# Optimization experiments

Hardware: AMD Instinct MI355X
Metric: run time of the kernel (lower is better)

The kernel has to match this reference:

```python
import jax, jax.numpy as jnp
import numpy as np

N = 100_000        # nodes
E = 3_200_000      # edges (avg degree 32)
D_IN = 512
D_HID = 512
D_OUT = 512
EPS = 1e-5         # BatchNorm1d eps


def _xavier(key, fan_out, fan_in, gain=1.414):
    a = gain * np.sqrt(6.0 / (fan_in + fan_out))
    return jax.random.uniform(key, (fan_out, fan_in), jnp.float32, -a, a)


def setup_inputs() -> dict:
    key = jax.random.key(0)
    ks = jax.random.split(key, 6)
    graph_node = jax.random.normal(ks[0], (N, D_IN), jnp.float32)
    edge_index = jax.random.randint(ks[1], (2, E), 0, N, dtype=jnp.int32)
    return {
        "graph_node": graph_node,
        "edge_index": edge_index,
        "W0": _xavier(ks[2], D_HID, D_IN),
        "b0": jnp.zeros((D_HID,), jnp.float32),
        "W1": _xavier(ks[3], D_HID, D_HID),
        "b1": jnp.zeros((D_HID,), jnp.float32),
        "W2": _xavier(ks[4], D_OUT, D_HID),
        "b2": jnp.zeros((D_OUT,), jnp.float32),
    }


def _gcn_scale(src, dst):
    # Faithful to torch gcn_conv: self-loops removed then re-added for all N
    # nodes; degree computed on dst; edge messages h[src]*w are scattered to
    # src (the cols tensor in the original is dead code). Hence the whole op
    # reduces to a per-node scale s[i] = sum_{out-edges of i} w + deg[i]^-1.
    mask = (src != dst).astype(jnp.float32)          # drop self-loops
    deg = jax.ops.segment_sum(mask, dst, num_segments=N) + 1.0  # +1 self-loop
    dinv = deg ** -0.5                               # deg >= 1, no inf
    w = dinv[src] * dinv[dst] * mask                 # [E]
    s = jax.ops.segment_sum(w, src, num_segments=N) + 1.0 / deg  # [N]
    return s


def _batchnorm(x):
    # BatchNorm1d(affine=False, track_running_stats=False): batch stats always
    mu = x.mean(axis=0)
    var = x.var(axis=0)  # biased variance, matches torch normalization
    return (x - mu) * jax.lax.rsqrt(var + EPS)


def reference(graph_node, edge_index, W0, b0, W1, b1, W2, b2):
    src, dst = edge_index[0], edge_index[1]
    s = _gcn_scale(src, dst)[:, None]                # [N,1], graph-only
    x = graph_node
    for W, b in ((W0, b0), (W1, b1)):
        x = (x @ W.T) * s + b                        # linear, gcn_conv, bias
        x = jax.nn.relu(_batchnorm(x))
        # dropout inactive at inference
    x = (x @ W2.T) * s + b2
    return x
```

## Files before the change

kernel.cpp:

```cpp
#include <hip/hip_runtime.h>

#define N_NODES 100000
#define N_EDGES 3200000
#define DIM 512
#define MPAD 100096
#define MTILES 782
#define BN_EPS 1e-5f

#define RBITS 14
#define NBINS 16384
#define NRANGE 8
#define NBLK 64
#define EDGES_PER_BLK (N_EDGES / NBLK)

typedef _Float16 half8 __attribute__((ext_vector_type(8)));
typedef float floatx4 __attribute__((ext_vector_type(4)));


__global__ __launch_bounds__(256) void convert_x_kernel(const float* __restrict__ x,
                                                        _Float16* __restrict__ out) {
    size_t idx = ((size_t)blockIdx.x * 256 + threadIdx.x) * 8;
    int row = (int)(idx >> 9);
    half8 h;
    if (row < N_NODES) {
        const float4* p = (const float4*)(x + idx);
        float4 a = p[0], b = p[1];
        h[0] = (_Float16)a.x; h[1] = (_Float16)a.y; h[2] = (_Float16)a.z; h[3] = (_Float16)a.w;
        h[4] = (_Float16)b.x; h[5] = (_Float16)b.y; h[6] = (_Float16)b.z; h[7] = (_Float16)b.w;
    } else {
        #pragma unroll
        for (int k = 0; k < 8; ++k) h[k] = (_Float16)0.0f;
    }
    *(half8*)(out + idx) = h;
}

__global__ __launch_bounds__(256) void convert_w_kernel(const float* __restrict__ in,
                                                        _Float16* __restrict__ out) {
    size_t idx = ((size_t)blockIdx.x * 256 + threadIdx.x) * 8;
    const float4* p = (const float4*)(in + idx);
    float4 a = p[0], b = p[1];
    half8 h;
    h[0] = (_Float16)a.x; h[1] = (_Float16)a.y; h[2] = (_Float16)a.z; h[3] = (_Float16)a.w;
    h[4] = (_Float16)b.x; h[5] = (_Float16)b.y; h[6] = (_Float16)b.z; h[7] = (_Float16)b.w;
    *(half8*)(out + idx) = h;
}


template <bool IS_DEG>
__global__ __launch_bounds__(256) void hist_stage1(const int* __restrict__ ei,
                                                   const float* __restrict__ dinv,
                                                   float* __restrict__ part) {
    __shared__ float bins[NBINS];
    const int tid = threadIdx.x;
    const int r = blockIdx.x & (NRANGE - 1);
    const int b = blockIdx.x >> 3;
    for (int i = tid; i < NBINS; i += 256) bins[i] = 0.f;
    __syncthreads();

    const int e0 = b * EDGES_PER_BLK;
    const int e1 = e0 + EDGES_PER_BLK;
    const int lo = r << RBITS;
    const int hi = lo + NBINS;
    for (int e = e0 + tid * 4; e < e1; e += 256 * 4) {
        int4 sv = *(const int4*)(ei + e);
        int4 dv = *(const int4*)(ei + N_EDGES + e);
        const int ss[4] = {sv.x, sv.y, sv.z, sv.w};
        const int dd[4] = {dv.x, dv.y, dv.z, dv.w};
        #pragma unroll
        for (int k = 0; k < 4; ++k) {
            const int s = ss[k], d = dd[k];
            if (s == d) continue;
            const int key = IS_DEG ? d : s;
            if (key >= lo && key < hi) {
                const float val = IS_DEG ? 1.0f : dinv[d];
                atomicAdd(&bins[key - lo], val);
            }
        }
    }
    __syncthreads();

    float* dst = part + (size_t)blockIdx.x * NBINS;
    for (int i = tid; i < NBINS; i += 256) dst[i] = bins[i];
}

__global__ __launch_bounds__(256) void hist_stage2_deg(const float* __restrict__ part,
                                                       float* __restrict__ dinv,
                                                       float* __restrict__ sarr) {
    const int i = blockIdx.x * 256 + threadIdx.x;
    if (i >= MPAD) return;
    const int r = i >> RBITS, bin = i & (NBINS - 1);
    float h = 0.f;
    #pragma unroll 8
    for (int b = 0; b < NBLK; ++b)
        h += part[(size_t)(b * NRANGE + r) * NBINS + bin];
    if (i < N_NODES) {
        const float deg = h + 1.0f;
        dinv[i] = rsqrtf(deg);
        sarr[i] = 1.0f / deg;
    } else {
        dinv[i] = 0.f;
        sarr[i] = 0.f;
    }
}

__global__ __launch_bounds__(256) void hist_stage2_s(const float* __restrict__ part,
                                                     const float* __restrict__ dinv,
                                                     float* __restrict__ sarr) {
    const int i = blockIdx.x * 256 + threadIdx.x;
    if (i >= MPAD) return;
    const int r = i >> RBITS, bin = i & (NBINS - 1);
    float t = 0.f;
    #pragma unroll 8
    for (int b = 0; b < NBLK; ++b)
        t += part[(size_t)(b * NRANGE + r) * NBINS + bin];
    if (i < N_NODES) sarr[i] += dinv[i] * t;
}


template <bool FINAL>
__global__ __launch_bounds__(256) void gemm_kernel(
    const _Float16* __restrict__ A,
    const _Float16* __restrict__ W,
    const float* __restrict__ sarr,
    const float* __restrict__ bias,
    void* __restrict__ out,
    float* __restrict__ colsum,
    float* __restrict__ colsq)
{
    __shared__ _Float16 As[128 * 32];
    __shared__ _Float16 Bs[128 * 32];
    __shared__ float lsum[128];
    __shared__ float lsq[128];

    const int tid  = threadIdx.x;
    const int wave = tid >> 6;
    const int lane = tid & 63;
    const int quad = lane >> 4;
    const int l16  = lane & 15;

    const int ct = blockIdx.x & 3;
    const int rt = blockIdx.x >> 2;
    const int m0 = rt * 128;
    const int n0 = ct * 128;
    const int wm = (wave >> 1) * 64;
    const int wn = (wave & 1) * 64;

    floatx4 acc[4][4];
    #pragma unroll
    for (int i = 0; i < 4; ++i)
        #pragma unroll
        for (int j = 0; j < 4; ++j)
            acc[i][j] = (floatx4){0.f, 0.f, 0.f, 0.f};

    const int f0 = wave * 1024 + lane * 16;
    const int ra = f0 >> 6;
    const int ca = f0 & 63;

    const char* Ab = (const char*)(A + (size_t)m0 * DIM) + ca;
    const char* Bb = (const char*)(W + (size_t)n0 * DIM) + ca;

    for (int kb = 0; kb < DIM; kb += 32) {
        #pragma unroll
        for (int is = 0; is < 2; ++is) {
            int r = is * 64 + ra;
            __builtin_amdgcn_global_load_lds(
                (const __attribute__((address_space(1))) void*)(Ab + (size_t)r * (DIM * 2) + kb * 2),
                (__attribute__((address_space(3))) void*)(As + is * 2048 + (f0 >> 1)),
                16, 0, 0);
            __builtin_amdgcn_global_load_lds(
                (const __attribute__((address_space(1))) void*)(Bb + (size_t)r * (DIM * 2) + kb * 2),
                (__attribute__((address_space(3))) void*)(Bs + is * 2048 + (f0 >> 1)),
                16, 0, 0);
        }
        __syncthreads();

        half8 af[4], bfr[4];
        #pragma unroll
        for (int i = 0; i < 4; ++i)
            af[i] = *(const half8*)(As + (wm + i * 16 + l16) * 32 + quad * 8);
        #pragma unroll
        for (int j = 0; j < 4; ++j)
            bfr[j] = *(const half8*)(Bs + (wn + j * 16 + l16) * 32 + quad * 8);

        #pragma unroll
        for (int i = 0; i < 4; ++i)
            #pragma unroll
            for (int j = 0; j < 4; ++j)
                acc[i][j] = __builtin_amdgcn_mfma_f32_16x16x32_f16(af[i], bfr[j], acc[i][j], 0, 0, 0);

        __syncthreads();
    }

    if (!FINAL) {
        if (tid < 128) { lsum[tid] = 0.f; lsq[tid] = 0.f; }
        __syncthreads();
    }

    float4 sva[4];
    #pragma unroll
    for (int i = 0; i < 4; ++i)
        sva[i] = *(const float4*)(sarr + m0 + wm + i * 16 + quad * 4);
    float bv[4];
    #pragma unroll
    for (int j = 0; j < 4; ++j)
        bv[j] = bias[n0 + wn + j * 16 + l16];

    #pragma unroll
    for (int j = 0; j < 4; ++j) {
        const int col_g = n0 + wn + j * 16 + l16;
        float cs = 0.f, cq = 0.f;
        #pragma unroll
        for (int i = 0; i < 4; ++i) {
            const int rbase = m0 + wm + i * 16 + quad * 4;
            #pragma unroll
            for (int r = 0; r < 4; ++r) {
                const int row_g = rbase + r;
                const float sval = ((const float*)&sva[i])[r];
                const float yv = acc[i][j][r] * sval + bv[j];
                if (FINAL) {
                    if (row_g < N_NODES)
                        ((float*)out)[(size_t)row_g * DIM + col_g] = yv;
                } else {
                    ((_Float16*)out)[(size_t)row_g * DIM + col_g] = (_Float16)yv;
                    if (row_g < N_NODES) { cs += yv; cq += yv * yv; }
                }
            }
        }
        if (!FINAL) {
            atomicAdd(&lsum[wn + j * 16 + l16], cs);
            atomicAdd(&lsq[wn + j * 16 + l16], cq);
        }
    }
    if (!FINAL) {
        __syncthreads();
        if (tid < 128) {
            atomicAdd(&colsum[n0 + tid], lsum[tid]);
            atomicAdd(&colsq[n0 + tid], lsq[tid]);
        }
    }
}


__global__ void bn_finalize(const float* __restrict__ colsum, const float* __restrict__ colsq,
                            float* __restrict__ mu, float* __restrict__ rstd) {
    int c = threadIdx.x;
    float m = colsum[c] * (1.0f / (float)N_NODES);
    float v = colsq[c] * (1.0f / (float)N_NODES) - m * m;
    mu[c] = m;
    rstd[c] = rsqrtf(v + BN_EPS);
}

__global__ __launch_bounds__(256) void bn_apply(_Float16* __restrict__ y,
                                                const float* __restrict__ mu,
                                                const float* __restrict__ rstd) {
    size_t idx = ((size_t)blockIdx.x * 256 + threadIdx.x) * 8;
    int row = (int)(idx >> 9);
    int col = (int)(idx & 511);
    half8 h;
    if (row < N_NODES) {
        h = *(const half8*)(y + idx);
        float4 m0 = *(const float4*)(mu + col);
        float4 m1 = *(const float4*)(mu + col + 4);
        float4 r0 = *(const float4*)(rstd + col);
        float4 r1 = *(const float4*)(rstd + col + 4);
        float mus[8] = {m0.x, m0.y, m0.z, m0.w, m1.x, m1.y, m1.z, m1.w};
        float rs[8]  = {r0.x, r0.y, r0.z, r0.w, r1.x, r1.y, r1.z, r1.w};
        #pragma unroll
        for (int k = 0; k < 8; ++k) {
            float v = ((float)h[k] - mus[k]) * rs[k];
            h[k] = (_Float16)fmaxf(v, 0.f);
        }
    } else {
        #pragma unroll
        for (int k = 0; k < 8; ++k) h[k] = (_Float16)0.0f;
    }
    *(half8*)(y + idx) = h;
}


extern "C" void kernel_launch(void* const* d_in, const int* in_sizes, int n_in,
                              void* d_out, int out_size, void* d_ws, size_t ws_size,
                              hipStream_t stream) {
    const float* graph_node = (const float*)d_in[0];
    const int*   edge_index = (const int*)d_in[1];
    const float* W0 = (const float*)d_in[2];
    const float* b0 = (const float*)d_in[3];
    const float* W1 = (const float*)d_in[4];
    const float* b1 = (const float*)d_in[5];
    const float* W2 = (const float*)d_in[6];
    const float* b2 = (const float*)d_in[7];

    char* ws = (char*)d_ws;
    const size_t XB = (size_t)MPAD * DIM * 2;
    _Float16* x0  = (_Float16*)ws;
    _Float16* wf  = (_Float16*)(ws + XB);
    float* dinv   = (float*)(ws + XB + 3 * DIM * DIM * 2);
    float* sarr   = dinv + MPAD;
    float* stats  = sarr + MPAD;
    float *sum0 = stats,        *sq0 = stats + 512,  *mu0 = stats + 1024, *rstd0 = stats + 1536;
    float *sum1 = stats + 2048, *sq1 = stats + 2560, *mu1 = stats + 3072, *rstd1 = stats + 3584;

    _Float16* x1 = (_Float16*)d_out;
    float* part = (float*)((char*)d_out + (size_t)110 * 1024 * 1024);

    hipMemsetAsync(stats, 0, 4096 * sizeof(float), stream);

    const int elemBlocks = MPAD * DIM / 8 / 256;
    convert_x_kernel<<<elemBlocks, 256, 0, stream>>>(graph_node, x0);
    convert_w_kernel<<<128, 256, 0, stream>>>(W0, wf);
    convert_w_kernel<<<128, 256, 0, stream>>>(W1, wf + 262144);
    convert_w_kernel<<<128, 256, 0, stream>>>(W2, wf + 524288);

    const int statBlocks = (MPAD + 255) / 256;
    hist_stage1<true><<<NRANGE * NBLK, 256, 0, stream>>>(edge_index, dinv, part);
    hist_stage2_deg<<<statBlocks, 256, 0, stream>>>(part, dinv, sarr);
    hist_stage1<false><<<NRANGE * NBLK, 256, 0, stream>>>(edge_index, dinv, part);
    hist_stage2_s<<<statBlocks, 256, 0, stream>>>(part, dinv, sarr);

    gemm_kernel<false><<<MTILES * 4, 256, 0, stream>>>(x0, wf, sarr, b0, x1, sum0, sq0);
    bn_finalize<<<1, 512, 0, stream>>>(sum0, sq0, mu0, rstd0);
    bn_apply<<<elemBlocks, 256, 0, stream>>>(x1, mu0, rstd0);

    gemm_kernel<false><<<MTILES * 4, 256, 0, stream>>>(x1, wf + 262144, sarr, b1, x0, sum1, sq1);
    bn_finalize<<<1, 512, 0, stream>>>(sum1, sq1, mu1, rstd1);
    bn_apply<<<elemBlocks, 256, 0, stream>>>(x0, mu1, rstd1);

    gemm_kernel<true><<<MTILES * 4, 256, 0, stream>>>(x0, wf + 524288, sarr, b2, d_out,
                                                      nullptr, nullptr);
}
```

Measured before the change: 938.5 us.

## Double-buffer GEMM LDS tiles and remap workgroup IDs across XCDs

The GEMM main loop now uses two LDS buffers, so the next K-slice is fetched with global_load_lds while MFMAs run on the current one, which halves the barriers per iteration. Workgroup indices in both the GEMM and the histogram kernel are permuted so that consecutive tiles land on the same XCD, improving L2 locality for the shared weight and edge data. The cost is double the LDS footprint, which may lower occupancy, and the remap assumes grid sizes divisible by 8.

```diff
diff --git a/kernel.cpp b/kernel.cpp
--- a/kernel.cpp
+++ b/kernel.cpp
@@ -52,8 +52,9 @@
                                                    float* __restrict__ part) {
     __shared__ float bins[NBINS];
     const int tid = threadIdx.x;
-    const int r = blockIdx.x & (NRANGE - 1);
-    const int b = blockIdx.x >> 3;
+    const int wg = (blockIdx.x & 7) * (NRANGE * NBLK / 8) + (blockIdx.x >> 3);
+    const int r = wg & (NRANGE - 1);
+    const int b = wg >> 3;
     for (int i = tid; i < NBINS; i += 256) bins[i] = 0.f;
     __syncthreads();
 
@@ -79,7 +80,7 @@
     }
     __syncthreads();
 
-    float* dst = part + (size_t)blockIdx.x * NBINS;
+    float* dst = part + (size_t)wg * NBINS;
     for (int i = tid; i < NBINS; i += 256) dst[i] = bins[i];
 }
 
@@ -127,8 +128,8 @@
     float* __restrict__ colsum,
     float* __restrict__ colsq)
 {
-    __shared__ _Float16 As[128 * 32];
-    __shared__ _Float16 Bs[128 * 32];
+    __shared__ _Float16 As[2][128 * 32];
+    __shared__ _Float16 Bs[2][128 * 32];
     __shared__ float lsum[128];
     __shared__ float lsq[128];
 
@@ -138,8 +139,9 @@
     const int quad = lane >> 4;
     const int l16  = lane & 15;
 
-    const int ct = blockIdx.x & 3;
-    const int rt = blockIdx.x >> 2;
+    const int wg = (blockIdx.x & 7) * (MTILES * 4 / 8) + (blockIdx.x >> 3);
+    const int ct = wg & 3;
+    const int rt = wg >> 2;
     const int m0 = rt * 128;
     const int n0 = ct * 128;
     const int wm = (wave >> 1) * 64;
@@ -159,37 +161,53 @@
     const char* Ab = (const char*)(A + (size_t)m0 * DIM) + ca;
     const char* Bb = (const char*)(W + (size_t)n0 * DIM) + ca;
 
-    for (int kb = 0; kb < DIM; kb += 32) {
+    auto stage = [&](int buf, int kb) {
         #pragma unroll
         for (int is = 0; is < 2; ++is) {
-            int r = is * 64 + ra;
+            const int r = is * 64 + ra;
             __builtin_amdgcn_global_load_lds(
                 (const __attribute__((address_space(1))) void*)(Ab + (size_t)r * (DIM * 2) + kb * 2),
-                (__attribute__((address_space(3))) void*)(As + is * 2048 + (f0 >> 1)),
+                (__attribute__((address_space(3))) void*)(&As[buf][is * 2048 + (f0 >> 1)]),
                 16, 0, 0);
             __builtin_amdgcn_global_load_lds(
                 (const __attribute__((address_space(1))) void*)(Bb + (size_t)r * (DIM * 2) + kb * 2),
-                (__attribute__((address_space(3))) void*)(Bs + is * 2048 + (f0 >> 1)),
+                (__attribute__((address_space(3))) void*)(&Bs[buf][is * 2048 + (f0 >> 1)]),
                 16, 0, 0);
         }
-        __syncthreads();
-
+    };
+
+    auto compute = [&](int buf) {
         half8 af[4], bfr[4];
         #pragma unroll
         for (int i = 0; i < 4; ++i)
-            af[i] = *(const half8*)(As + (wm + i * 16 + l16) * 32 + quad * 8);
+            af[i] = *(const half8*)(&As[buf][(wm + i * 16 + l16) * 32 + quad * 8]);
         #pragma unroll
         for (int j = 0; j < 4; ++j)
-            bfr[j] = *(const half8*)(Bs + (wn + j * 16 + l16) * 32 + quad * 8);
-
+            bfr[j] = *(const half8*)(&Bs[buf][(wn + j * 16 + l16) * 32 + quad * 8]);
         #pragma unroll
         for (int i = 0; i < 4; ++i)
             #pragma unroll
             for (int j = 0; j < 4; ++j)
                 acc[i][j] = __builtin_amdgcn_mfma_f32_16x16x32_f16(af[i], bfr[j], acc[i][j], 0, 0, 0);
-
+    };
+
+    stage(0, 0);
+    __syncthreads();
+
+    int kb = 32;
+    for (int it = 0; it < 7; ++it) {
+        stage(1, kb);
+        compute(0);
         __syncthreads();
-    }
+        stage(0, kb + 32);
+        compute(1);
+        __syncthreads();
+        kb += 64;
+    }
+    stage(1, kb);
+    compute(0);
+    __syncthreads();
+    compute(1);
 
     if (!FINAL) {
         if (tid < 128) { lsum[tid] = 0.f; lsq[tid] = 0.f; }
```

After: 903.2 us. -3.8%, faster.

## Rewrite GEMM as 256x256 double-buffered pipelined tile with XCD-aware block mapping

Applied to the files above, without the earlier changes.

Replaces the 128x128 single-buffered GEMM with a 512-thread, 256x256 tile kernel that double-buffers K-slices in LDS and interleaves async global-to-LDS loads with MFMA phases, using explicit waitcnt, barriers and setprio. LDS reads use an XOR swizzle to avoid bank conflicts, and workgroups are remapped so consecutive tiles land on the same XCD for L2 reuse. The histogram kernel also gets an XCD-aware block remap. The aim is to hide memory latency and raise MFMA utilisation, at the cost of higher register and LDS pressure and fragile hand-tuned scheduling.

```diff
diff --git a/kernel.cpp b/kernel.cpp
--- a/kernel.cpp
+++ b/kernel.cpp
@@ -4,8 +4,10 @@
 #define N_EDGES 3200000
 #define DIM 512
 #define MPAD 100096
-#define MTILES 782
 #define BN_EPS 1e-5f
+
+#define GRTILES 391
+#define GGRID 782
 
 #define RBITS 14
 #define NBINS 16384
@@ -52,8 +54,9 @@
                                                    float* __restrict__ part) {
     __shared__ float bins[NBINS];
     const int tid = threadIdx.x;
-    const int r = blockIdx.x & (NRANGE - 1);
-    const int b = blockIdx.x >> 3;
+    const int wg = (blockIdx.x & 7) * (NRANGE * NBLK / 8) + (blockIdx.x >> 3);
+    const int r = wg & (NRANGE - 1);
+    const int b = wg >> 3;
     for (int i = tid; i < NBINS; i += 256) bins[i] = 0.f;
     __syncthreads();
 
@@ -79,7 +82,7 @@
     }
     __syncthreads();
 
-    float* dst = part + (size_t)blockIdx.x * NBINS;
+    float* dst = part + (size_t)wg * NBINS;
     for (int i = tid; i < NBINS; i += 256) dst[i] = bins[i];
 }
 
@@ -117,8 +120,70 @@
 }
 
 
+#define BARRIER __builtin_amdgcn_s_barrier()
+#define WAIT_LGKM do { asm volatile("s_waitcnt lgkmcnt(0)" ::: "memory"); \
+                       __builtin_amdgcn_sched_barrier(0); } while (0)
+#define VM2 do { asm volatile("s_waitcnt vmcnt(2)" ::: "memory"); \
+                 __builtin_amdgcn_sched_barrier(0); } while (0)
+#define VM0 do { asm volatile("s_waitcnt vmcnt(0)" ::: "memory"); \
+                 __builtin_amdgcn_sched_barrier(0); } while (0)
+#define VM8 do { asm volatile("s_waitcnt vmcnt(8)" ::: "memory"); \
+                 __builtin_amdgcn_sched_barrier(0); } while (0)
+#define VNONE ((void)0)
+#define PRIO1 __builtin_amdgcn_s_setprio(1)
+#define PRIO0 __builtin_amdgcn_s_setprio(0)
+
+#define STG(buf, ab, h, kt) do { \
+    const char* _s = (ab) ? Bsrc : Asrc; \
+    __builtin_amdgcn_global_load_lds( \
+        (const __attribute__((address_space(1))) void*)(_s + (size_t)((h)*128 + rowS0)*1024 + (kt)*128 + cbS), \
+        (__attribute__((address_space(3))) void*)(&smem[buf][ab][h][tid*8]), 16, 0, 0); \
+    __builtin_amdgcn_global_load_lds( \
+        (const __attribute__((address_space(1))) void*)(_s + (size_t)((h)*128 + rowS0 + 64)*1024 + (kt)*128 + cbS), \
+        (__attribute__((address_space(3))) void*)(&smem[buf][ab][h][4096 + tid*8]), 16, 0, 0); \
+} while (0)
+
+#define RDA(base, i0) do { \
+    _Pragma("unroll") for (int ii = 0; ii < 4; ++ii) \
+        _Pragma("unroll") for (int s = 0; s < 2; ++s) \
+            fa[ii][s] = *(const half8*)((const char*)(base) + ((i0) + ii) * 2048 + s * 1024 + inb); \
+} while (0)
+
+#define RDB(base, j0) do { \
+    _Pragma("unroll") for (int jj = 0; jj < 2; ++jj) \
+        _Pragma("unroll") for (int s = 0; s < 2; ++s) \
+            fb[(j0) + jj][s] = *(const half8*)((const char*)(base) + (brow0 + (j0) + jj) * 2048 + s * 1024 + inb); \
+} while (0)
+
+#define MM(i0, j0) do { \
+    _Pragma("unroll") for (int s = 0; s < 2; ++s) \
+        _Pragma("unroll") for (int ii = 0; ii < 4; ++ii) \
+            _Pragma("unroll") for (int jj = 0; jj < 2; ++jj) \
+                acc[(i0)+ii][(j0)+jj] = __builtin_amdgcn_mfma_f32_16x16x32_f16( \
+                    fa[ii][s], fb[(j0)+jj][s], acc[(i0)+ii][(j0)+jj], 0, 0, 0); \
+} while (0)
+
+#define ITER(S13, S47, S8, KTA, KTB, KTC, VMP4, VMP8) do { \
+     RDA(Ab0, 0); RDB(Bb0, 0); if (S13) STG(1, 0, 1, KTA); \
+              BARRIER; WAIT_LGKM; PRIO1; MM(0, 0); PRIO0; BARRIER; \
+     RDB(Bb0, 2); if (S13) STG(1, 1, 0, KTA); \
+              BARRIER; WAIT_LGKM; PRIO1; MM(0, 2); PRIO0; BARRIER; \
+     RDA(Ab0, 4); if (S13) STG(1, 1, 1, KTA); \
+              BARRIER; WAIT_LGKM; PRIO1; MM(4, 0); PRIO0; BARRIER; \
+     if (S47) STG(0, 0, 0, KTB); \
+              BARRIER; PRIO1; MM(4, 2); PRIO0; VMP4; BARRIER; \
+     RDA(Ab1, 0); RDB(Bb1, 0); if (S47) STG(0, 0, 1, KTB); \
+              BARRIER; WAIT_LGKM; PRIO1; MM(0, 0); PRIO0; BARRIER; \
+     RDB(Bb1, 2); if (S47) STG(0, 1, 0, KTB); \
+              BARRIER; WAIT_LGKM; PRIO1; MM(0, 2); PRIO0; BARRIER; \
+     RDA(Ab1, 4); if (S47) STG(0, 1, 1, KTB); \
+              BARRIER; WAIT_LGKM; PRIO1; MM(4, 0); PRIO0; BARRIER; \
+     if (S8) STG(1, 0, 0, KTC); \
+              BARRIER; PRIO1; MM(4, 2); PRIO0; VMP8; BARRIER; \
+} while (0)
+
 template <bool FINAL>
-__global__ __launch_bounds__(256) void gemm_kernel(
+__global__ __launch_bounds__(512, 2) void gemm_kernel(
     const _Float16* __restrict__ A,
     const _Float16* __restrict__ W,
     const float* __restrict__ sarr,
@@ -127,10 +192,7 @@
     float* __restrict__ colsum,
     float* __restrict__ colsq)
 {
-    __shared__ _Float16 As[128 * 32];
-    __shared__ _Float16 Bs[128 * 32];
-    __shared__ float lsum[128];
-    __shared__ float lsq[128];
+    __shared__ _Float16 smem[2][2][2][8192];
 
     const int tid  = threadIdx.x;
     const int wave = tid >> 6;
@@ -138,85 +200,75 @@
     const int quad = lane >> 4;
     const int l16  = lane & 15;
 
-    const int ct = blockIdx.x & 3;
-    const int rt = blockIdx.x >> 2;
-    const int m0 = rt * 128;
-    const int n0 = ct * 128;
-    const int wm = (wave >> 1) * 64;
-    const int wn = (wave & 1) * 64;
-
-    floatx4 acc[4][4];
+    const int xcd = blockIdx.x & 7, bidx = blockIdx.x >> 3;
+    const int qq = 97, rr = 6;
+    const int wg = (xcd < rr ? xcd * (qq + 1) : rr * (qq + 1) + (xcd - rr) * qq) + bidx;
+    const int ct = wg & 1, rt = wg >> 1;
+    const int m0 = rt * 256, n0 = ct * 256;
+
+    const int wmh   = wave >> 2;
+    const int wnq   = wave & 3;
+    const int bhalf = (wave >> 1) & 1;
+    const int brow0 = (wave & 1) * 4;
+
+    const _Float16* Ab0 = &smem[0][0][wmh][0];
+    const _Float16* Ab1 = &smem[1][0][wmh][0];
+    const _Float16* Bb0 = &smem[0][1][bhalf][0];
+    const _Float16* Bb1 = &smem[1][1][bhalf][0];
+
+    const int inb = (l16 * 64 + quad * 16) ^ (((l16 >> 3) & 1) << 5);
+
+    const int st0 = tid >> 6;
+    int bsw = (tid & 63) * 16;
+    bsw ^= ((bsw >> 9) & 1) << 5;
+    const int rowS0 = ((st0 >> 1) << 4) + (bsw >> 6);
+    const int cbS   = ((st0 & 1) << 6) + (bsw & 63);
+
+    const char* Asrc = (const char*)(A + (size_t)m0 * DIM);
+    const char* Bsrc = (const char*)(W + (size_t)n0 * DIM);
+
+    floatx4 acc[8][4];
     #pragma unroll
-    for (int i = 0; i < 4; ++i)
+    for (int i = 0; i < 8; ++i)
         #pragma unroll
         for (int j = 0; j < 4; ++j)
             acc[i][j] = (floatx4){0.f, 0.f, 0.f, 0.f};
 
-    const int f0 = wave * 1024 + lane * 16;
-    const int ra = f0 >> 6;
-    const int ca = f0 & 63;
-
-    const char* Ab = (const char*)(A + (size_t)m0 * DIM) + ca;
-    const char* Bb = (const char*)(W + (size_t)n0 * DIM) + ca;
-
-    for (int kb = 0; kb < DIM; kb += 32) {
-        #pragma unroll
-        for (int is = 0; is < 2; ++is) {
-            int r = is * 64 + ra;
-            __builtin_amdgcn_global_load_lds(
-                (const __attribute__((address_space(1))) void*)(Ab + (size_t)r * (DIM * 2) + kb * 2),
-                (__attribute__((address_space(3))) void*)(As + is * 2048 + (f0 >> 1)),
-                16, 0, 0);
-            __builtin_amdgcn_global_load_lds(
-                (const __attribute__((address_space(1))) void*)(Bb + (size_t)r * (DIM * 2) + kb * 2),
-                (__attribute__((address_space(3))) void*)(Bs + is * 2048 + (f0 >> 1)),
-                16, 0, 0);
-        }
+    half8 fa[4][2];
+    half8 fb[4][2];
+
+    STG(0, 0, 0, 0); STG(0, 0, 1, 0); STG(0, 1, 0, 0); STG(0, 1, 1, 0);
+    STG(1, 0, 0, 1); STG(1, 0, 1, 1); STG(1, 1, 0, 1); STG(1, 1, 1, 1);
+    VM8;
+    BARRIER;
+
+    ITER(false, true,  true,  1, 2, 3, VM2, VM2);
+    ITER(true,  true,  true,  3, 4, 5, VM2, VM2);
+    ITER(true,  true,  true,  5, 6, 7, VM2, VM2);
+    ITER(true,  false, false, 7, 0, 0, VM0, VNONE);
+
+    float* lsum = (float*)&smem[0][0][0][0];
+    float* lsq  = lsum + 256;
+    if (!FINAL) {
+        if (tid < 256) { lsum[tid] = 0.f; lsq[tid] = 0.f; }
         __syncthreads();
-
-        half8 af[4], bfr[4];
-        #pragma unroll
-        for (int i = 0; i < 4; ++i)
-            af[i] = *(const half8*)(As + (wm + i * 16 + l16) * 32 + quad * 8);
-        #pragma unroll
-        for (int j = 0; j < 4; ++j)
-            bfr[j] = *(const half8*)(Bs + (wn + j * 16 + l16) * 32 + quad * 8);
-
-        #pragma unroll
-        for (int i = 0; i < 4; ++i)
-            #pragma unroll
-            for (int j = 0; j < 4; ++j)
-                acc[i][j] = __builtin_amdgcn_mfma_f32_16x16x32_f16(af[i], bfr[j], acc[i][j], 0, 0, 0);
-
-        __syncthreads();
-    }
-
-    if (!FINAL) {
-        if (tid < 128) { lsum[tid] = 0.f; lsq[tid] = 0.f; }
-        __syncthreads();
-    }
-
-    float4 sva[4];
-    #pragma unroll
-    for (int i = 0; i < 4; ++i)
-        sva[i] = *(const float4*)(sarr + m0 + wm + i * 16 + quad * 4);
-    float bv[4];
-    #pragma unroll
-    for (int j = 0; j < 4; ++j)
-        bv[j] = bias[n0 + wn + j * 16 + l16];
-
+    }
+
+    const int crow0 = m0 + wmh * 128;
+    const int ccol0 = n0 + wnq * 64;
     #pragma unroll
     for (int j = 0; j < 4; ++j) {
-        const int col_g = n0 + wn + j * 16 + l16;
+        const int col_g = ccol0 + j * 16 + l16;
+        const float bv = bias[col_g];
         float cs = 0.f, cq = 0.f;
         #pragma unroll
-        for (int i = 0; i < 4; ++i) {
-            const int rbase = m0 + wm + i * 16 + quad * 4;
+        for (int i = 0; i < 8; ++i) {
+            const int rbase = crow0 + i * 16 + quad * 4;
+            const float4 sv = *(const float4*)(sarr + rbase);
             #pragma unroll
-            for (int r = 0; r < 4; ++r) {
-                const int row_g = rbase + r;
-                const float sval = ((const float*)&sva[i])[r];
-                const float yv = acc[i][j][r] * sval + bv[j];
+            for (int r2 = 0; r2 < 4; ++r2) {
+                const int row_g = rbase + r2;
+                const float yv = acc[i][j][r2] * ((const float*)&sv)[r2] + bv;
                 if (FINAL) {
                     if (row_g < N_NODES)
                         ((float*)out)[(size_t)row_g * DIM + col_g] = yv;
@@ -227,13 +279,13 @@
             }
         }
         if (!FINAL) {
-            atomicAdd(&lsum[wn + j * 16 + l16], cs);
-            atomicAdd(&lsq[wn + j * 16 + l16], cq);
+            atomicAdd(&lsum[wnq * 64 + j * 16 + l16], cs);
+            atomicAdd(&lsq[wnq * 64 + j * 16 + l16], cq);
         }
     }
     if (!FINAL) {
         __syncthreads();
-        if (tid < 128) {
+        if (tid < 256) {
             atomicAdd(&colsum[n0 + tid], lsum[tid]);
             atomicAdd(&colsq[n0 + tid], lsq[tid]);
         }
@@ -317,14 +369,14 @@
     hist_stage1<false><<<NRANGE * NBLK, 256, 0, stream>>>(edge_index, dinv, part);
     hist_stage2_s<<<statBlocks, 256, 0, stream>>>(part, dinv, sarr);
 
-    gemm_kernel<false><<<MTILES * 4, 256, 0, stream>>>(x0, wf, sarr, b0, x1, sum0, sq0);
+    gemm_kernel<false><<<GGRID, 512, 0, stream>>>(x0, wf, sarr, b0, x1, sum0, sq0);
     bn_finalize<<<1, 512, 0, stream>>>(sum0, sq0, mu0, rstd0);
     bn_apply<<<elemBlocks, 256, 0, stream>>>(x1, mu0, rstd0);
 
-    gemm_kernel<false><<<MTILES * 4, 256, 0, stream>>>(x1, wf + 262144, sarr, b1, x0, sum1, sq1);
+    gemm_kernel<false><<<GGRID, 512, 0, stream>>>(x1, wf + 262144, sarr, b1, x0, sum1, sq1);
     bn_finalize<<<1, 512, 0, stream>>>(sum1, sq1, mu1, rstd1);
     bn_apply<<<elemBlocks, 256, 0, stream>>>(x0, mu1, rstd1);
 
-    gemm_kernel<true><<<MTILES * 4, 256, 0, stream>>>(x0, wf + 524288, sarr, b2, d_out,
-                                                      nullptr, nullptr);
-}
+    gemm_kernel<true><<<GGRID, 512, 0, stream>>>(x0, wf + 524288, sarr, b2, d_out,
+                                                 nullptr, nullptr);
+}
```

Measured after the change: 857.1 us. -8.7%, faster.

## Restructure GEMM to keep weight slab in LDS and stream A from global

Applied to the files above, without the earlier changes.

The GEMM now uses 512-thread blocks covering a 512x64 output tile. Each block loads the full 64x512 weight slice into swizzled LDS once, and every wave reads its A fragments directly from global memory with no per-k-step LDS staging or barriers. Block IDs are remapped so that consecutive blocks spread across XCDs, in both the GEMM and the histogram kernels. This removes the per-iteration __syncthreads and A staging, but A loads from global are now uncoalesced-ish fragment reads, each A row tile is re-read by 8 column blocks, and the large LDS footprint limits occupancy.

```diff
diff --git a/kernel.cpp b/kernel.cpp
--- a/kernel.cpp
+++ b/kernel.cpp
@@ -4,8 +4,13 @@
 #define N_EDGES 3200000
 #define DIM 512
 #define MPAD 100096
-#define MTILES 782
 #define BN_EPS 1e-5f
+
+#define GBM 512
+#define GBN 64
+#define GMT 196
+#define GNT 8
+#define GGRID (GMT * GNT)
 
 #define RBITS 14
 #define NBINS 16384
@@ -52,8 +57,9 @@
                                                    float* __restrict__ part) {
     __shared__ float bins[NBINS];
     const int tid = threadIdx.x;
-    const int r = blockIdx.x & (NRANGE - 1);
-    const int b = blockIdx.x >> 3;
+    const int wg = (blockIdx.x & 7) * (NRANGE * NBLK / 8) + (blockIdx.x >> 3);
+    const int r = wg & (NRANGE - 1);
+    const int b = wg >> 3;
     for (int i = tid; i < NBINS; i += 256) bins[i] = 0.f;
     __syncthreads();
 
@@ -79,7 +85,7 @@
     }
     __syncthreads();
 
-    float* dst = part + (size_t)blockIdx.x * NBINS;
+    float* dst = part + (size_t)wg * NBINS;
     for (int i = tid; i < NBINS; i += 256) dst[i] = bins[i];
 }
 
@@ -118,7 +124,7 @@
 
 
 template <bool FINAL>
-__global__ __launch_bounds__(256) void gemm_kernel(
+__global__ __launch_bounds__(512, 4) void gemm_kernel(
     const _Float16* __restrict__ A,
     const _Float16* __restrict__ W,
     const float* __restrict__ sarr,
@@ -127,10 +133,9 @@
     float* __restrict__ colsum,
     float* __restrict__ colsq)
 {
-    __shared__ _Float16 As[128 * 32];
-    __shared__ _Float16 Bs[128 * 32];
-    __shared__ float lsum[128];
-    __shared__ float lsq[128];
+    __shared__ _Float16 Wl[GBN * DIM];
+    __shared__ float lsum[GBN];
+    __shared__ float lsq[GBN];
 
     const int tid  = threadIdx.x;
     const int wave = tid >> 6;
@@ -138,12 +143,24 @@
     const int quad = lane >> 4;
     const int l16  = lane & 15;
 
-    const int ct = blockIdx.x & 3;
-    const int rt = blockIdx.x >> 2;
-    const int m0 = rt * 128;
-    const int n0 = ct * 128;
-    const int wm = (wave >> 1) * 64;
-    const int wn = (wave & 1) * 64;
+    const int wg = (blockIdx.x & 7) * GMT + (blockIdx.x >> 3);
+    const int ct = wg & 7;
+    const int rt = wg >> 3;
+    const int m0 = rt * GBM;
+    const int n0 = ct * GBN;
+
+    {
+        const char* Wsrc = (const char*)(W + (size_t)n0 * DIM);
+        const int inswz = (lane * 16) ^ (wave << 4);
+        #pragma unroll
+        for (int it = 0; it < 8; ++it) {
+            __builtin_amdgcn_global_load_lds(
+                (const __attribute__((address_space(1))) void*)(Wsrc + (it * 8 + wave) * 1024 + inswz),
+                (__attribute__((address_space(3))) void*)(Wl + it * 4096 + tid * 8),
+                16, 0, 0);
+        }
+    }
+    __syncthreads();
 
     floatx4 acc[4][4];
     #pragma unroll
@@ -152,88 +169,66 @@
         for (int j = 0; j < 4; ++j)
             acc[i][j] = (floatx4){0.f, 0.f, 0.f, 0.f};
 
-    const int f0 = wave * 1024 + lane * 16;
-    const int ra = f0 >> 6;
-    const int ca = f0 & 63;
-
-    const char* Ab = (const char*)(A + (size_t)m0 * DIM) + ca;
-    const char* Bb = (const char*)(W + (size_t)n0 * DIM) + ca;
-
-    for (int kb = 0; kb < DIM; kb += 32) {
-        #pragma unroll
-        for (int is = 0; is < 2; ++is) {
-            int r = is * 64 + ra;
-            __builtin_amdgcn_global_load_lds(
-                (const __attribute__((address_space(1))) void*)(Ab + (size_t)r * (DIM * 2) + kb * 2),
-                (__attribute__((address_space(3))) void*)(As + is * 2048 + (f0 >> 1)),
-                16, 0, 0);
-            __builtin_amdgcn_global_load_lds(
-                (const __attribute__((address_space(1))) void*)(Bb + (size_t)r * (DIM * 2) + kb * 2),
-                (__attribute__((address_space(3))) void*)(Bs + is * 2048 + (f0 >> 1)),
-                16, 0, 0);
-        }
-        __syncthreads();
-
-        half8 af[4], bfr[4];
-        #pragma unroll
-        for (int i = 0; i < 4; ++i)
-            af[i] = *(const half8*)(As + (wm + i * 16 + l16) * 32 + quad * 8);
+    const char* Arow = (const char*)A + (size_t)(m0 + wave * 64 + l16) * (DIM * 2) + quad * 16;
+    const int swz = (l16 & 7) << 4;
+    const char* Wb = (const char*)Wl + (size_t)l16 * 1024;
+
+    #pragma unroll 4
+    for (int ks = 0; ks < 16; ++ks) {
+        const int kb2 = ks * 64;
+        half8 fa[4], fb[4];
         #pragma unroll
         for (int j = 0; j < 4; ++j)
-            bfr[j] = *(const half8*)(Bs + (wn + j * 16 + l16) * 32 + quad * 8);
-
-        #pragma unroll
-        for (int i = 0; i < 4; ++i)
+            fb[j] = *(const half8*)(Wb + j * 16384 + ((kb2 + quad * 16) ^ swz));
+        #pragma unroll
+        for (int sub = 0; sub < 4; ++sub)
+            fa[sub] = *(const half8*)(Arow + sub * 16 * (DIM * 2) + kb2);
+        #pragma unroll
+        for (int sub = 0; sub < 4; ++sub)
             #pragma unroll
             for (int j = 0; j < 4; ++j)
-                acc[i][j] = __builtin_amdgcn_mfma_f32_16x16x32_f16(af[i], bfr[j], acc[i][j], 0, 0, 0);
-
+                acc[sub][j] = __builtin_amdgcn_mfma_f32_16x16x32_f16(fa[sub], fb[j], acc[sub][j], 0, 0, 0);
+    }
+
+    if (!FINAL) {
         __syncthreads();
-    }
-
-    if (!FINAL) {
-        if (tid < 128) { lsum[tid] = 0.f; lsq[tid] = 0.f; }
+        if (tid < GBN) { lsum[tid] = 0.f; lsq[tid] = 0.f; }
         __syncthreads();
     }
 
-    float4 sva[4];
-    #pragma unroll
-    for (int i = 0; i < 4; ++i)
-        sva[i] = *(const float4*)(sarr + m0 + wm + i * 16 + quad * 4);
-    float bv[4];
-    #pragma unroll
-    for (int j = 0; j < 4; ++j)
-        bv[j] = bias[n0 + wn + j * 16 + l16];
-
+    const int crow0 = m0 + wave * 64;
     #pragma unroll
     for (int j = 0; j < 4; ++j) {
-        const int col_g = n0 + wn + j * 16 + l16;
+        const int col_g = n0 + j * 16 + l16;
+        const float bv = bias[col_g];
         float cs = 0.f, cq = 0.f;
         #pragma unroll
-        for (int i = 0; i < 4; ++i) {
-            const int rbase = m0 + wm + i * 16 + quad * 4;
+        for (int sub = 0; sub < 4; ++sub) {
+            const int rbase = crow0 + sub * 16 + quad * 4;
+            const float4 sv = *(const float4*)(sarr + rbase);
             #pragma unroll
-            for (int r = 0; r < 4; ++r) {
-                const int row_g = rbase + r;
-                const float sval = ((const float*)&sva[i])[r];
-                const float yv = acc[i][j][r] * sval + bv[j];
+            for (int r2 = 0; r2 < 4; ++r2) {
+                const int row_g = rbase + r2;
+                const float yv = acc[sub][j][r2] * ((const float*)&sv)[r2] + bv;
                 if (FINAL) {
                     if (row_g < N_NODES)
                         ((float*)out)[(size_t)row_g * DIM + col_g] = yv;
                 } else {
-                    ((_Float16*)out)[(size_t)row_g * DIM + col_g] = (_Float16)yv;
-                    if (row_g < N_NODES) { cs += yv; cq += yv * yv; }
+                    if (row_g < N_NODES) {
+                        ((_Float16*)out)[(size_t)row_g * DIM + col_g] = (_Float16)yv;
+                        cs += yv; cq += yv * yv;
+                    }
                 }
             }
         }
         if (!FINAL) {
-            atomicAdd(&lsum[wn + j * 16 + l16], cs);
-            atomicAdd(&lsq[wn + j * 16 + l16], cq);
+            atomicAdd(&lsum[j * 16 + l16], cs);
+            atomicAdd(&lsq[j * 16 + l16], cq);
         }
     }
     if (!FINAL) {
         __syncthreads();
-        if (tid < 128) {
+        if (tid < GBN) {
             atomicAdd(&colsum[n0 + tid], lsum[tid]);
             atomicAdd(&colsq[n0 + tid], lsq[tid]);
         }
@@ -317,14 +312,14 @@
     hist_stage1<false><<<NRANGE * NBLK, 256, 0, stream>>>(edge_index, dinv, part);
     hist_stage2_s<<<statBlocks, 256, 0, stream>>>(part, dinv, sarr);
 
-    gemm_kernel<false><<<MTILES * 4, 256, 0, stream>>>(x0, wf, sarr, b0, x1, sum0, sq0);
+    gemm_kernel<false><<<GGRID, 512, 0, stream>>>(x0, wf, sarr, b0, x1, sum0, sq0);
     bn_finalize<<<1, 512, 0, stream>>>(sum0, sq0, mu0, rstd0);
     bn_apply<<<elemBlocks, 256, 0, stream>>>(x1, mu0, rstd0);
 
-    gemm_kernel<false><<<MTILES * 4, 256, 0, stream>>>(x1, wf + 262144, sarr, b1, x0, sum1, sq1);
+    gemm_kernel<false><<<GGRID, 512, 0, stream>>>(x1, wf + 262144, sarr, b1, x0, sum1, sq1);
     bn_finalize<<<1, 512, 0, stream>>>(sum1, sq1, mu1, rstd1);
     bn_apply<<<elemBlocks, 256, 0, stream>>>(x0, mu1, rstd1);
 
-    gemm_kernel<true><<<MTILES * 4, 256, 0, stream>>>(x0, wf + 524288, sarr, b2, d_out,
-                                                      nullptr, nullptr);
-}
+    gemm_kernel<true><<<GGRID, 512, 0, stream>>>(x0, wf + 524288, sarr, b2, d_out,
+                                                 nullptr, nullptr);
+}
```

Measured after the change: 1.004 ms. +7.0%, slower.
